# Kernel optimization log

Hardware: AMD Instinct MI355X
Metric: run time of the kernel (lower is better)

Reference implementation:

```python
import jax, jax.numpy as jnp
import numpy as np

B, IN_DIM, HIDDEN, N_CLASSES, D_Z = 16384, 1024, 2048, 8, 256
LN_EPS = 1e-5  # torch.nn.LayerNorm default


def _l2_normalize(x, axis=1, eps=1e-12):
    # matches F.normalize: x / max(||x||, eps)
    n = jnp.sqrt(jnp.sum(x * x, axis=axis, keepdims=True))
    return x / jnp.maximum(n, eps)


def setup_inputs() -> dict:
    key = jax.random.key(0)
    ks = jax.random.split(key, 9)
    s1 = 1.0 / np.sqrt(IN_DIM)
    s2 = 1.0 / np.sqrt(HIDDEN)
    return {
        "feat": jax.random.normal(ks[0], (B, IN_DIM), dtype=jnp.float32),
        "z_cat": jax.random.normal(ks[1], (B, D_Z), dtype=jnp.float32),
        "mu_cat": jax.random.normal(ks[2], (N_CLASSES, D_Z), dtype=jnp.float32),
        "ln_gamma": jnp.ones((N_CLASSES, IN_DIM), dtype=jnp.float32),
        "ln_beta": jnp.zeros((N_CLASSES, IN_DIM), dtype=jnp.float32),
        "W1": jax.random.uniform(ks[3], (N_CLASSES, IN_DIM, HIDDEN), jnp.float32, -s1, s1),
        "b1": jax.random.uniform(ks[4], (N_CLASSES, HIDDEN), jnp.float32, -s1, s1),
        "W2": jax.random.uniform(ks[5], (N_CLASSES, HIDDEN, N_CLASSES), jnp.float32, -s2, s2),
        "b2": jax.random.uniform(ks[6], (N_CLASSES, N_CLASSES), jnp.float32, -s2, s2),
        "tau_gate": 1,
    }


def reference(feat, z_cat, mu_cat, ln_gamma, ln_beta, W1, b1, W2, b2, tau_gate):
    # --- cosine-similarity softmax gate ---
    zn = _l2_normalize(z_cat, axis=1)            # [B, Dz]
    mun = _l2_normalize(mu_cat, axis=1)          # [E, Dz]
    sims = zn @ mun.T                            # [B, E]
    tau = max(1e-6, float(tau_gate))
    w = jax.nn.softmax(sims / tau, axis=1)       # [B, E]

    # --- batched experts: LN -> Linear -> ReLU -> (Dropout=identity, eval) -> Linear ---
    mu = jnp.mean(feat, axis=-1, keepdims=True)
    var = jnp.mean(jnp.square(feat - mu), axis=-1, keepdims=True)
    xhat = (feat - mu) * jax.lax.rsqrt(var + LN_EPS)            # [B, D] (shared)
    x_e = xhat[None] * ln_gamma[:, None, :] + ln_beta[:, None, :]  # [E, B, D]
    h = jax.nn.relu(jnp.einsum('ebd,edh->ebh', x_e, W1) + b1[:, None, :])  # [E, B, H]
    exp_logits = jnp.einsum('ebh,ehc->ebc', h, W2) + b2[:, None, :]        # [E, B, C]

    # --- gate-weighted sum over experts ---
    logits = jnp.einsum('ebc,be->bc', exp_logits, w)  # [B, C]
    return logits, w
```

## Files before the change

kernel.cpp:

```cpp
#include <hip/hip_runtime.h>
#include <hip/hip_bf16.h>
#include <cstdint>

#define NB     16384
#define DIN    1024
#define HID    2048
#define NE     8
#define NC     8
#define DZ     256

#define BM     256
#define BNB    128
#define BK     64
#define KSTEPS (DIN/BK)
#define NUNITS 2048
#define GRID_MAIN 512

typedef short bf16x8 __attribute__((ext_vector_type(8)));
typedef float f32x4  __attribute__((ext_vector_type(4)));

__device__ __forceinline__ unsigned short f2bf(float f) {
    unsigned int u = __float_as_uint(f);
    unsigned int r = (u + 0x7FFFu + ((u >> 16) & 1u)) >> 16;
    return (unsigned short)r;
}

__device__ __forceinline__ void async_copy16(const void* g, void* l) {
    __builtin_amdgcn_global_load_lds(
        (const __attribute__((address_space(1))) unsigned int*)g,
        (__attribute__((address_space(3))) unsigned int*)l, 16, 0, 0);
}

__global__ __launch_bounds__(256) void k_gate(const float* __restrict__ z,
                                              const float* __restrict__ mu,
                                              const int* __restrict__ tau_i,
                                              const float* __restrict__ b2,
                                              float* __restrict__ wout,
                                              float* __restrict__ logits) {
    int row = blockIdx.x * 4 + (threadIdx.x >> 6);
    int l = threadIdx.x & 63;
    float4 zv = *(const float4*)&z[(size_t)row * DZ + l * 4];
    float zz = zv.x * zv.x + zv.y * zv.y + zv.z * zv.z + zv.w * zv.w;
    float dots[NE], mm[NE];
#pragma unroll
    for (int e = 0; e < NE; ++e) {
        float4 m = *(const float4*)&mu[e * DZ + l * 4];
        dots[e] = zv.x * m.x + zv.y * m.y + zv.z * m.z + zv.w * m.w;
        mm[e]   = m.x * m.x + m.y * m.y + m.z * m.z + m.w * m.w;
    }
#pragma unroll
    for (int off = 32; off; off >>= 1) {
        zz += __shfl_xor(zz, off);
#pragma unroll
        for (int e = 0; e < NE; ++e) {
            dots[e] += __shfl_xor(dots[e], off);
            mm[e]   += __shfl_xor(mm[e], off);
        }
    }
    float zn = fmaxf(sqrtf(zz), 1e-12f);
    float tau = fmaxf(1e-6f, (float)tau_i[0]);
    float s[NE], mx = -1e30f;
#pragma unroll
    for (int e = 0; e < NE; ++e) {
        s[e] = dots[e] / (zn * fmaxf(sqrtf(mm[e]), 1e-12f)) / tau;
        mx = fmaxf(mx, s[e]);
    }
    float sum = 0.f;
#pragma unroll
    for (int e = 0; e < NE; ++e) { s[e] = expf(s[e] - mx); sum += s[e]; }
    float inv = 1.f / sum;
    if (l < NE) {
        wout[(size_t)row * NE + l] = s[l] * inv;
        float acc = 0.f;
#pragma unroll
        for (int e = 0; e < NE; ++e) acc += s[e] * inv * b2[e * NC + l];
        logits[(size_t)row * NC + l] = acc;
    }
}

__global__ __launch_bounds__(256) void k_ln(const float* __restrict__ feat,
                                            unsigned short* __restrict__ xhat) {
    int row = blockIdx.x;
    int t = threadIdx.x;
    float4 v = *(const float4*)&feat[(size_t)row * DIN + t * 4];
    float s  = v.x + v.y + v.z + v.w;
    float sq = v.x * v.x + v.y * v.y + v.z * v.z + v.w * v.w;
#pragma unroll
    for (int off = 32; off; off >>= 1) {
        s  += __shfl_down(s, off);
        sq += __shfl_down(sq, off);
    }
    __shared__ float ls[8];
    int w = t >> 6, l = t & 63;
    if (l == 0) { ls[w] = s; ls[4 + w] = sq; }
    __syncthreads();
    s  = ls[0] + ls[1] + ls[2] + ls[3];
    sq = ls[4] + ls[5] + ls[6] + ls[7];
    float mean = s * (1.f / DIN);
    float var  = sq * (1.f / DIN) - mean * mean;
    float r = 1.0f / sqrtf(var + 1e-5f);
    uint2 p;
    p.x = (unsigned)f2bf((v.x - mean) * r) | ((unsigned)f2bf((v.y - mean) * r) << 16);
    p.y = (unsigned)f2bf((v.z - mean) * r) | ((unsigned)f2bf((v.w - mean) * r) << 16);
    *(uint2*)&xhat[(size_t)row * DIN + t * 4] = p;
}

__global__ __launch_bounds__(256) void k_w2prep(const float* __restrict__ W2,
                                                const float* __restrict__ b1,
                                                unsigned short* __restrict__ w2t,
                                                float* __restrict__ b1p,
                                                int* __restrict__ qcounter) {
    int i = blockIdx.x * 256 + threadIdx.x;
    if (i == 0) qcounter[0] = 0;
    int e = i >> 15;
    int rem = i & 32767;
    int c = rem >> 11;
    int h = rem & 2047;
    float v = (c < NC) ? W2[((size_t)(e * HID + h)) * NC + c] : 0.f;
    w2t[i] = f2bf(v);
    if (i < NE * HID) b1p[i] = b1[i];
}

__global__ __launch_bounds__(256) void k_w1prep(const float* __restrict__ W1,
                                                const float* __restrict__ gamma,
                                                const float* __restrict__ beta,
                                                unsigned short* __restrict__ w1t,
                                                float* __restrict__ b1p) {
    __shared__ float tile[64][65];
    int e  = blockIdx.z;
    int d0 = blockIdx.y * 64;
    int h0 = blockIdx.x * 64;
    int tx = threadIdx.x & 15, ty = threadIdx.x >> 4;
#pragma unroll
    for (int rr = 0; rr < 4; ++rr) {
        int d = ty + rr * 16;
        float4 v = *(const float4*)&W1[((size_t)e * DIN + d0 + d) * HID + h0 + tx * 4];
        tile[tx * 4 + 0][d] = v.x;
        tile[tx * 4 + 1][d] = v.y;
        tile[tx * 4 + 2][d] = v.z;
        tile[tx * 4 + 3][d] = v.w;
    }
    __syncthreads();
    float4 g = *(const float4*)&gamma[(size_t)e * DIN + d0 + tx * 4];
#pragma unroll
    for (int rr = 0; rr < 4; ++rr) {
        int h = ty + rr * 16;
        uint2 p;
        p.x = (unsigned)f2bf(tile[h][tx * 4 + 0] * g.x) |
              ((unsigned)f2bf(tile[h][tx * 4 + 1] * g.y) << 16);
        p.y = (unsigned)f2bf(tile[h][tx * 4 + 2] * g.z) |
              ((unsigned)f2bf(tile[h][tx * 4 + 3] * g.w) << 16);
        *(uint2*)&w1t[((size_t)e * HID + h0 + h) * DIN + d0 + tx * 4] = p;
    }
    if (threadIdx.x < 64) {
        int h = threadIdx.x;
        float sacc = 0.f;
        for (int r = 0; r < 64; ++r)
            sacc += beta[(size_t)e * DIN + d0 + r] * tile[h][r];
        atomicAdd(&b1p[(size_t)e * HID + h0 + h], sacc);
    }
}

__global__ __launch_bounds__(256, 2) void moe_main(
        const unsigned short* __restrict__ xhat,
        const unsigned short* __restrict__ w1t,
        const float* __restrict__ b1p,
        const unsigned short* __restrict__ w2t,
        const float* __restrict__ wg,
        float* __restrict__ logits,
        int* __restrict__ qcounter) {
    __shared__ __align__(16) short lds_a[BM * BK];
    __shared__ __align__(16) short lds_b[BNB * BK];
    __shared__ __align__(16) char  lds_ht[4 * 64 * 80];
    __shared__ int s_u;

    const int t = threadIdx.x;
    const int w = t >> 6, l = t & 63;
    const int q = l >> 4, ml = l & 15;
    const int wm = (w >> 1) * 128;
    const int wn = (w & 1) * 64;

    const int strow  = w * 8 + (l >> 3);
    const int kslot8 = (((l & 7) ^ ((l >> 3) & 7))) * 8;
    const int rswz   = ml & 7;
    char* myht = lds_ht + w * 5120;

    for (;;) {
        if (t == 0) s_u = atomicAdd(qcounter, 1);
        __syncthreads();
        const int u = s_u;
        if (u >= NUNITS) break;
        const int btile = u & 127;
        const int e     = (u >> 7) & 7;
        const int half  = u >> 10;
        const int b0 = btile * BNB;
        const unsigned short* gA = w1t + (size_t)e * HID * DIN;
        const unsigned short* gB = xhat + (size_t)b0 * DIN;

        f32x4 acc2[4];
#pragma unroll
        for (int tb = 0; tb < 4; ++tb) acc2[tb] = (f32x4){0.f, 0.f, 0.f, 0.f};

        for (int ch = half * 4; ch < half * 4 + 4; ++ch) {
            const int hid0 = ch * BM;
            f32x4 acc[8][4];
#pragma unroll
            for (int i = 0; i < 8; ++i)
#pragma unroll
                for (int j = 0; j < 4; ++j) acc[i][j] = (f32x4){0.f, 0.f, 0.f, 0.f};

            for (int ks = 0; ks < KSTEPS; ++ks) {
                const int k0 = ks * BK;
#pragma unroll
                for (int it = 0; it < 8; ++it) {
                    const int row = it * 32 + strow;
                    async_copy16(gA + (size_t)(hid0 + row) * DIN + k0 + kslot8,
                                 (char*)lds_a + it * 4096 + w * 1024 + (l << 4));
                    if (it < 4)
                        async_copy16(gB + (size_t)row * DIN + k0 + kslot8,
                                     (char*)lds_b + it * 4096 + w * 1024 + (l << 4));
                }
                __syncthreads();
#pragma unroll 1
                for (int kk = 0; kk < 2; ++kk) {
                    const int cswz = ((kk * 4 + q) ^ rswz) * 8;
                    bf16x8 bF[4];
#pragma unroll
                    for (int j = 0; j < 4; ++j)
                        bF[j] = *(const bf16x8*)&lds_b[(wn + 16 * j + ml) * BK + cswz];
#pragma unroll
                    for (int i = 0; i < 8; ++i) {
                        const bf16x8 aF =
                            *(const bf16x8*)&lds_a[(wm + 16 * i + ml) * BK + cswz];
#pragma unroll
                        for (int j = 0; j < 4; ++j)
                            acc[i][j] = __builtin_amdgcn_mfma_f32_16x16x32_bf16(
                                aF, bF[j], acc[i][j], 0, 0, 0);
                    }
                }
                __syncthreads();
            }

#pragma unroll
            for (int s = 0; s < 4; ++s) {
#pragma unroll
                for (int i2 = 0; i2 < 2; ++i2) {
                    const int i = 2 * s + i2;
                    const float4 bias = *(const float4*)
                        &b1p[(size_t)e * HID + hid0 + wm + 16 * i + 4 * q];
#pragma unroll
                    for (int j = 0; j < 4; ++j) {
                        float v0 = fmaxf(acc[i][j].x + bias.x, 0.f);
                        float v1 = fmaxf(acc[i][j].y + bias.y, 0.f);
                        float v2 = fmaxf(acc[i][j].z + bias.z, 0.f);
                        float v3 = fmaxf(acc[i][j].w + bias.w, 0.f);
                        uint2 p;
                        p.x = (unsigned)f2bf(v0) | ((unsigned)f2bf(v1) << 16);
                        p.y = (unsigned)f2bf(v2) | ((unsigned)f2bf(v3) << 16);
                        const int brow = 16 * j + ml;
                        *(uint2*)(myht + brow * 80 + (16 * i2 + 4 * q) * 2) = p;
                    }
                }
                const bf16x8 b2f = *(const bf16x8*)&w2t[((size_t)e * 16 + ml) * HID +
                                                        hid0 + wm + 32 * s + 8 * q];
#pragma unroll
                for (int tb = 0; tb < 4; ++tb) {
                    const bf16x8 a2f =
                        *(const bf16x8*)(myht + (16 * tb + ml) * 80 + q * 16);
                    acc2[tb] = __builtin_amdgcn_mfma_f32_16x16x32_bf16(
                        a2f, b2f, acc2[tb], 0, 0, 0);
                }
            }
        }

        __syncthreads();
        float* red = (float*)lds_ht;
        if (w >= 2) {
            float* dst = red + ((size_t)((w & 1) * 64 + l)) * 16;
#pragma unroll
            for (int tb = 0; tb < 4; ++tb)
#pragma unroll
                for (int r = 0; r < 4; ++r) dst[tb * 4 + r] = acc2[tb][r];
        }
        __syncthreads();
        if (w < 2) {
            const float* src = red + ((size_t)((w & 1) * 64 + l)) * 16;
            const int c = ml;
            if (c < NC) {
#pragma unroll
                for (int tb = 0; tb < 4; ++tb) {
#pragma unroll
                    for (int r = 0; r < 4; ++r) {
                        float v = acc2[tb][r] + src[tb * 4 + r];
                        const int bg = b0 + wn + 16 * tb + 4 * q + r;
                        const float wgt = wg[(size_t)bg * NE + e];
                        atomicAdd(&logits[(size_t)bg * NC + c], wgt * v);
                    }
                }
            }
        }
    }
}

extern "C" void kernel_launch(void* const* d_in, const int* in_sizes, int n_in,
                              void* d_out, int out_size, void* d_ws, size_t ws_size,
                              hipStream_t stream) {
    const float* feat  = (const float*)d_in[0];
    const float* z     = (const float*)d_in[1];
    const float* mu    = (const float*)d_in[2];
    const float* gamma = (const float*)d_in[3];
    const float* beta  = (const float*)d_in[4];
    const float* W1    = (const float*)d_in[5];
    const float* b1    = (const float*)d_in[6];
    const float* W2    = (const float*)d_in[7];
    const float* b2    = (const float*)d_in[8];
    const int*   tau   = (const int*)d_in[9];

    float* logits = (float*)d_out;
    float* wout   = logits + (size_t)NB * NC;

    char* ws = (char*)d_ws;
    unsigned short* xhat = (unsigned short*)ws;
    unsigned short* w1t  = (unsigned short*)(ws + 33554432);
    unsigned short* w2t  = (unsigned short*)(ws + 67108864);
    float*          b1p  = (float*)(ws + 67633152);
    int*            qcnt = (int*)(ws + 67698688);

    k_gate<<<NB / 4, 256, 0, stream>>>(z, mu, tau, b2, wout, logits);
    k_ln<<<NB, 256, 0, stream>>>(feat, xhat);
    k_w2prep<<<(NE * 16 * HID) / 256, 256, 0, stream>>>(W2, b1, w2t, b1p, qcnt);
    k_w1prep<<<dim3(HID / 64, DIN / 64, NE), 256, 0, stream>>>(W1, gamma, beta, w1t, b1p);
    moe_main<<<dim3(GRID_MAIN), 256, 0, stream>>>(xhat, w1t, b1p, w2t,
                                                  wout, logits, qcnt);
}
```

Baseline: 725.0 us.

## Use 256x256 GEMM tiles with static tile assignment instead of atomic work queue

The main MoE kernel now computes square 256x256 output tiles, each warp holding a 128x128 accumulator. Previously a block covered 256 hidden units by 128 batch rows and looped over four hidden chunks. The dynamic atomic work counter is replaced by a static round-robin mapping of tiles to blocks. The aim is better operand reuse per LDS load and more MFMA work per barrier. In exchange, the 256 accumulator registers per thread threaten occupancy and spilling, and each tile now issues more atomic adds to logits for its partial second-layer sums.

After: 2.837 ms. 291% more time.

```diff
diff --git a/kernel.cpp b/kernel.cpp
--- a/kernel.cpp
+++ b/kernel.cpp
@@ -9,12 +9,14 @@
 #define NC     8
 #define DZ     256
 
-#define BM     256
-#define BNB    128
+#define MT     256
+#define NT     256
 #define BK     64
 #define KSTEPS (DIN/BK)
-#define NUNITS 2048
+#define MTILES (NE*HID/MT)
+#define NTILES (NB/NT)
 #define GRID_MAIN 512
+#define UPB    ((MTILES*NTILES)/GRID_MAIN)
 
 typedef short bf16x8 __attribute__((ext_vector_type(8)));
 typedef float f32x4  __attribute__((ext_vector_type(4)));
@@ -108,10 +110,8 @@
 __global__ __launch_bounds__(256) void k_w2prep(const float* __restrict__ W2,
                                                 const float* __restrict__ b1,
                                                 unsigned short* __restrict__ w2t,
-                                                float* __restrict__ b1p,
-                                                int* __restrict__ qcounter) {
+                                                float* __restrict__ b1p) {
     int i = blockIdx.x * 256 + threadIdx.x;
-    if (i == 0) qcounter[0] = 0;
     int e = i >> 15;
     int rem = i & 32767;
     int c = rem >> 11;
@@ -167,132 +167,128 @@
         const float* __restrict__ b1p,
         const unsigned short* __restrict__ w2t,
         const float* __restrict__ wg,
-        float* __restrict__ logits,
-        int* __restrict__ qcounter) {
-    __shared__ __align__(16) short lds_a[BM * BK];
-    __shared__ __align__(16) short lds_b[BNB * BK];
-    __shared__ __align__(16) char  lds_ht[4 * 64 * 80];
-    __shared__ int s_u;
+        float* __restrict__ logits) {
+    __shared__ __align__(16) char lds_raw[65536];
+    short* lds_a = (short*)lds_raw;
+    short* lds_b = (short*)(lds_raw + 32768);
 
     const int t = threadIdx.x;
     const int w = t >> 6, l = t & 63;
     const int q = l >> 4, ml = l & 15;
     const int wm = (w >> 1) * 128;
-    const int wn = (w & 1) * 64;
+    const int wn = (w & 1) * 128;
 
     const int strow  = w * 8 + (l >> 3);
     const int kslot8 = (((l & 7) ^ ((l >> 3) & 7))) * 8;
     const int rswz   = ml & 7;
-    char* myht = lds_ht + w * 5120;
-
-    for (;;) {
-        if (t == 0) s_u = atomicAdd(qcounter, 1);
+    char* myht = lds_raw + w * 10240;
+    float* red = (float*)(lds_raw + 40960);
+
+    for (int un = 0; un < UPB; ++un) {
+        const int u = un * GRID_MAIN + blockIdx.x;
+        const int mtile = u & (MTILES - 1);
+        const int ntile = u >> 6;
+        const int e      = mtile >> 3;
+        const int hidOff = (mtile & 7) * MT;
+        const int b0 = ntile * NT;
+        const unsigned short* gA = w1t + (size_t)mtile * MT * DIN;
+        const unsigned short* gB = xhat + (size_t)b0 * DIN;
+
         __syncthreads();
-        const int u = s_u;
-        if (u >= NUNITS) break;
-        const int btile = u & 127;
-        const int e     = (u >> 7) & 7;
-        const int half  = u >> 10;
-        const int b0 = btile * BNB;
-        const unsigned short* gA = w1t + (size_t)e * HID * DIN;
-        const unsigned short* gB = xhat + (size_t)b0 * DIN;
-
-        f32x4 acc2[4];
-#pragma unroll
-        for (int tb = 0; tb < 4; ++tb) acc2[tb] = (f32x4){0.f, 0.f, 0.f, 0.f};
-
-        for (int ch = half * 4; ch < half * 4 + 4; ++ch) {
-            const int hid0 = ch * BM;
-            f32x4 acc[8][4];
-#pragma unroll
-            for (int i = 0; i < 8; ++i)
-#pragma unroll
-                for (int j = 0; j < 4; ++j) acc[i][j] = (f32x4){0.f, 0.f, 0.f, 0.f};
-
-            for (int ks = 0; ks < KSTEPS; ++ks) {
-                const int k0 = ks * BK;
-#pragma unroll
-                for (int it = 0; it < 8; ++it) {
-                    const int row = it * 32 + strow;
-                    async_copy16(gA + (size_t)(hid0 + row) * DIN + k0 + kslot8,
-                                 (char*)lds_a + it * 4096 + w * 1024 + (l << 4));
-                    if (it < 4)
-                        async_copy16(gB + (size_t)row * DIN + k0 + kslot8,
-                                     (char*)lds_b + it * 4096 + w * 1024 + (l << 4));
+
+        f32x4 acc[8][8];
+#pragma unroll
+        for (int i = 0; i < 8; ++i)
+#pragma unroll
+            for (int j = 0; j < 8; ++j) acc[i][j] = (f32x4){0.f, 0.f, 0.f, 0.f};
+
+        for (int ks = 0; ks < KSTEPS; ++ks) {
+            const int k0 = ks * BK;
+#pragma unroll
+            for (int it = 0; it < 8; ++it) {
+                const int row = it * 32 + strow;
+                async_copy16(gA + (size_t)row * DIN + k0 + kslot8,
+                             (char*)lds_a + it * 4096 + w * 1024 + (l << 4));
+                async_copy16(gB + (size_t)row * DIN + k0 + kslot8,
+                             (char*)lds_b + it * 4096 + w * 1024 + (l << 4));
+            }
+            __syncthreads();
+#pragma unroll 1
+            for (int kk = 0; kk < 2; ++kk) {
+                const int cswz = ((kk * 4 + q) ^ rswz) * 8;
+                bf16x8 bF[8];
+#pragma unroll
+                for (int j = 0; j < 8; ++j)
+                    bF[j] = *(const bf16x8*)&lds_b[(wn + 16 * j + ml) * BK + cswz];
+#pragma unroll
+                for (int i = 0; i < 8; ++i) {
+                    const bf16x8 aF =
+                        *(const bf16x8*)&lds_a[(wm + 16 * i + ml) * BK + cswz];
+#pragma unroll
+                    for (int j = 0; j < 8; ++j)
+                        acc[i][j] = __builtin_amdgcn_mfma_f32_16x16x32_bf16(
+                            aF, bF[j], acc[i][j], 0, 0, 0);
                 }
-                __syncthreads();
-#pragma unroll 1
-                for (int kk = 0; kk < 2; ++kk) {
-                    const int cswz = ((kk * 4 + q) ^ rswz) * 8;
-                    bf16x8 bF[4];
-#pragma unroll
-                    for (int j = 0; j < 4; ++j)
-                        bF[j] = *(const bf16x8*)&lds_b[(wn + 16 * j + ml) * BK + cswz];
-#pragma unroll
-                    for (int i = 0; i < 8; ++i) {
-                        const bf16x8 aF =
-                            *(const bf16x8*)&lds_a[(wm + 16 * i + ml) * BK + cswz];
-#pragma unroll
-                        for (int j = 0; j < 4; ++j)
-                            acc[i][j] = __builtin_amdgcn_mfma_f32_16x16x32_bf16(
-                                aF, bF[j], acc[i][j], 0, 0, 0);
-                    }
+            }
+            __syncthreads();
+        }
+
+        f32x4 acc2[8];
+#pragma unroll
+        for (int tb = 0; tb < 8; ++tb) acc2[tb] = (f32x4){0.f, 0.f, 0.f, 0.f};
+
+#pragma unroll
+        for (int s = 0; s < 4; ++s) {
+#pragma unroll
+            for (int i2 = 0; i2 < 2; ++i2) {
+                const int i = 2 * s + i2;
+                const float4 bias = *(const float4*)
+                    &b1p[(size_t)e * HID + hidOff + wm + 16 * i + 4 * q];
+#pragma unroll
+                for (int j = 0; j < 8; ++j) {
+                    float v0 = fmaxf(acc[i][j].x + bias.x, 0.f);
+                    float v1 = fmaxf(acc[i][j].y + bias.y, 0.f);
+                    float v2 = fmaxf(acc[i][j].z + bias.z, 0.f);
+                    float v3 = fmaxf(acc[i][j].w + bias.w, 0.f);
+                    uint2 p;
+                    p.x = (unsigned)f2bf(v0) | ((unsigned)f2bf(v1) << 16);
+                    p.y = (unsigned)f2bf(v2) | ((unsigned)f2bf(v3) << 16);
+                    const int brow = 16 * j + ml;
+                    *(uint2*)(myht + brow * 80 + (16 * i2 + 4 * q) * 2) = p;
                 }
-                __syncthreads();
-            }
-
-#pragma unroll
-            for (int s = 0; s < 4; ++s) {
-#pragma unroll
-                for (int i2 = 0; i2 < 2; ++i2) {
-                    const int i = 2 * s + i2;
-                    const float4 bias = *(const float4*)
-                        &b1p[(size_t)e * HID + hid0 + wm + 16 * i + 4 * q];
-#pragma unroll
-                    for (int j = 0; j < 4; ++j) {
-                        float v0 = fmaxf(acc[i][j].x + bias.x, 0.f);
-                        float v1 = fmaxf(acc[i][j].y + bias.y, 0.f);
-                        float v2 = fmaxf(acc[i][j].z + bias.z, 0.f);
-                        float v3 = fmaxf(acc[i][j].w + bias.w, 0.f);
-                        uint2 p;
-                        p.x = (unsigned)f2bf(v0) | ((unsigned)f2bf(v1) << 16);
-                        p.y = (unsigned)f2bf(v2) | ((unsigned)f2bf(v3) << 16);
-                        const int brow = 16 * j + ml;
-                        *(uint2*)(myht + brow * 80 + (16 * i2 + 4 * q) * 2) = p;
-                    }
-                }
-                const bf16x8 b2f = *(const bf16x8*)&w2t[((size_t)e * 16 + ml) * HID +
-                                                        hid0 + wm + 32 * s + 8 * q];
-#pragma unroll
-                for (int tb = 0; tb < 4; ++tb) {
-                    const bf16x8 a2f =
-                        *(const bf16x8*)(myht + (16 * tb + ml) * 80 + q * 16);
-                    acc2[tb] = __builtin_amdgcn_mfma_f32_16x16x32_bf16(
-                        a2f, b2f, acc2[tb], 0, 0, 0);
-                }
+            }
+            const bf16x8 b2f = *(const bf16x8*)&w2t[((size_t)e * 16 + ml) * HID +
+                                                    hidOff + wm + 32 * s + 8 * q];
+#pragma unroll
+            for (int tb = 0; tb < 8; ++tb) {
+                const bf16x8 a2f =
+                    *(const bf16x8*)(myht + (16 * tb + ml) * 80 + q * 16);
+                acc2[tb] = __builtin_amdgcn_mfma_f32_16x16x32_bf16(
+                    a2f, b2f, acc2[tb], 0, 0, 0);
             }
         }
 
         __syncthreads();
-        float* red = (float*)lds_ht;
         if (w >= 2) {
-            float* dst = red + ((size_t)((w & 1) * 64 + l)) * 16;
-#pragma unroll
-            for (int tb = 0; tb < 4; ++tb)
-#pragma unroll
-                for (int r = 0; r < 4; ++r) dst[tb * 4 + r] = acc2[tb][r];
+            float* dst = red + (size_t)(w & 1) * 2048;
+#pragma unroll
+            for (int tb = 0; tb < 8; ++tb)
+#pragma unroll
+                for (int r = 0; r < 4; ++r)
+                    dst[(16 * tb + 4 * q + r) * 16 + ml] = acc2[tb][r];
         }
         __syncthreads();
         if (w < 2) {
-            const float* src = red + ((size_t)((w & 1) * 64 + l)) * 16;
+            const float* src = red + (size_t)(w & 1) * 2048;
             const int c = ml;
             if (c < NC) {
 #pragma unroll
-                for (int tb = 0; tb < 4; ++tb) {
+                for (int tb = 0; tb < 8; ++tb) {
 #pragma unroll
                     for (int r = 0; r < 4; ++r) {
-                        float v = acc2[tb][r] + src[tb * 4 + r];
-                        const int bg = b0 + wn + 16 * tb + 4 * q + r;
+                        const int bl = 16 * tb + 4 * q + r;
+                        float v = acc2[tb][r] + src[bl * 16 + ml];
+                        const int bg = b0 + wn + bl;
                         const float wgt = wg[(size_t)bg * NE + e];
                         atomicAdd(&logits[(size_t)bg * NC + c], wgt * v);
                     }
@@ -324,12 +320,11 @@
     unsigned short* w1t  = (unsigned short*)(ws + 33554432);
     unsigned short* w2t  = (unsigned short*)(ws + 67108864);
     float*          b1p  = (float*)(ws + 67633152);
-    int*            qcnt = (int*)(ws + 67698688);
 
     k_gate<<<NB / 4, 256, 0, stream>>>(z, mu, tau, b2, wout, logits);
     k_ln<<<NB, 256, 0, stream>>>(feat, xhat);
-    k_w2prep<<<(NE * 16 * HID) / 256, 256, 0, stream>>>(W2, b1, w2t, b1p, qcnt);
+    k_w2prep<<<(NE * 16 * HID) / 256, 256, 0, stream>>>(W2, b1, w2t, b1p);
     k_w1prep<<<dim3(HID / 64, DIN / 64, NE), 256, 0, stream>>>(W1, gamma, beta, w1t, b1p);
     moe_main<<<dim3(GRID_MAIN), 256, 0, stream>>>(xhat, w1t, b1p, w2t,
-                                                  wout, logits, qcnt);
-}
+                                                  wout, logits);
+}
```
